# Kernel tuning notes

Hardware: AMD Instinct MI355X
Metric: run time of the kernel (lower is better)

Reference implementation:

```python
import jax, jax.numpy as jnp
import numpy as np
import math

N = 65536   # number of tree nodes
K = 4       # branching factor of the complete K-ary tree
D = 300     # input_size
H = 256     # hidden_size

def _levels(n, k):
    # complete k-ary tree: level l spans [start, start + k**l)
    levels, start, size = [], 0, 1
    while start < n:
        end = min(start + size, n)
        levels.append((start, end))
        start, size = end, size * k
    return levels

LEVELS = _levels(N, K)

def setup_inputs() -> dict:
    key = jax.random.key(0)
    ks = jax.random.split(key, 16)
    def U(k, shape, s):
        return jax.random.uniform(k, shape, jnp.float32, -s, s)
    s1 = 1.0 / math.sqrt(D + H)
    sfi = 1.0 / math.sqrt(D)
    sfh = 1.0 / math.sqrt(H)
    return {
        "inputs": jax.random.normal(ks[0], (N, D), jnp.float32),
        "ix_w": U(ks[1], (H, D), s1), "ix_b": U(ks[2], (H,), s1),
        "ih_w": U(ks[3], (H, H), s1), "ih_b": U(ks[4], (H,), s1),
        "ux_w": U(ks[5], (H, D), s1), "ux_b": U(ks[6], (H,), s1),
        "uh_w": U(ks[7], (H, H), s1), "uh_b": U(ks[8], (H,), s1),
        "fi_w": U(ks[9], (H, D), sfi), "fi_b": U(ks[10], (H,), sfi),
        "fh_w": U(ks[11], (H, H), sfh), "fh_b": U(ks[12], (H,), sfh),
    }

def reference(inputs, ix_w, ix_b, ih_w, ih_b, ux_w, ux_b, uh_w, uh_b,
              fi_w, fi_b, fh_w, fh_b):
    # Precompute all input projections once (batched over every node).
    ix = inputs @ ix_w.T + ix_b   # [N, H]
    ux = inputs @ ux_w.T + ux_b   # [N, H]
    fi = inputs @ fi_w.T + fi_b   # [N, H]
    h = jnp.zeros((N, H), inputs.dtype)
    c = jnp.zeros((N, H), inputs.dtype)
    # Bottom-up over tree levels (children before parents); level bounds static.
    for (s, e) in reversed(LEVELS):
        node = jnp.arange(s, e)                                   # [L]
        cidx = node[:, None] * K + 1 + jnp.arange(K)[None, :]     # [L, K]
        valid = cidx < N
        cidx = jnp.where(valid, cidx, 0)
        m = valid[..., None].astype(inputs.dtype)                 # [L, K, 1]
        hc = h[cidx] * m                                          # [L, K, H]
        cc = c[cidx] * m
        h_sum = hc.sum(axis=1)                                    # [L, H]
        # per-child forget gate: sigmoid(W_fi x + b_fi + W_fh h_k + b_fh)
        f = jax.nn.sigmoid(fi[s:e][:, None, :]
                           + jnp.einsum('lkh,gh->lkg', hc, fh_w) + fh_b)
        fc = (f * cc).sum(axis=1)                                 # masked via cc
        i = jax.nn.sigmoid(ix[s:e] + h_sum @ ih_w.T + ih_b)
        u = jnp.tanh(ux[s:e] + h_sum @ uh_w.T + uh_b)
        c_new = i * u + fc
        h_new = jnp.tanh(c_new)          # no output gate in this module
        h = h.at[s:e].set(h_new)
        c = c.at[s:e].set(c_new)
    # root node state (matches (next_h, [next_h, next_c]) at the root)
    return h[0], c[0]
```

## Files before the change

### kernel.cpp

```cpp
#include <hip/hip_runtime.h>


#define NTOT 65536
#define DD   300
#define KP   320
#define HH   256
#define LEAF_START 16384

typedef unsigned short u16;
typedef unsigned int   u32;
typedef __attribute__((ext_vector_type(8))) short bf16x8;
typedef __attribute__((ext_vector_type(4))) float f32x4;

#define OFF_HB    0ull
#define OFF_C     33554944ull
#define OFF_PRE   100664832ull
#define OFF_WXB   125830656ull
#define OFF_WHB   126322176ull
#define OFF_UNION 126715392ull
#define OFF_XB    (OFF_UNION)
#define OFF_PIU   (OFF_UNION)
#define OFF_PF    (OFF_UNION + 11272192ull)
#define OFF_HSUM  (OFF_UNION + 33685504ull)

__device__ __forceinline__ float sigm(float x) { return 1.f / (1.f + __expf(-x)); }
__device__ __forceinline__ float ftanh(float x) {
    x = fminf(15.f, fmaxf(-15.f, x));
    float e = __expf(2.f * x);
    return (e - 1.f) / (e + 1.f);
}
__device__ __forceinline__ u16 f2bf(float f) {
    union { float f; u32 u; } v; v.f = f;
    u32 r = v.u + 0x7fffu + ((v.u >> 16) & 1u);
    return (u16)(r >> 16);
}
__device__ __forceinline__ float bf2f(u16 b) {
    union { u32 u; float f; } v; v.u = ((u32)b) << 16;
    return v.f;
}

__global__ __launch_bounds__(256) void zero_pad(u16* __restrict__ hb,
                                                float* __restrict__ c) {
    const int t = threadIdx.x;
    hb[(size_t)NTOT * HH + t] = 0;
    c [(size_t)NTOT * HH + t] = 0.f;
}

__global__ __launch_bounds__(256) void conv_x(const float* __restrict__ X,
                                              u32* __restrict__ Xb2) {
    const size_t total = (size_t)NTOT * (KP / 2);
    for (size_t id = (size_t)blockIdx.x * 256 + threadIdx.x; id < total;
         id += (size_t)gridDim.x * 256) {
        const int node = (int)(id / (KP / 2));
        const int k    = ((int)(id % (KP / 2))) * 2;
        const float f0 = (k < DD)     ? X[(size_t)node * DD + k]     : 0.f;
        const float f1 = (k + 1 < DD) ? X[(size_t)node * DD + k + 1] : 0.f;
        Xb2[id] = (u32)f2bf(f0) | ((u32)f2bf(f1) << 16);
    }
}

__global__ __launch_bounds__(256) void conv_wx(const float* __restrict__ ixw,
                                               const float* __restrict__ uxw,
                                               const float* __restrict__ fiw,
                                               u32* __restrict__ W2) {
    const int total = 768 * (KP / 2);
    for (int id = blockIdx.x * 256 + threadIdx.x; id < total;
         id += gridDim.x * 256) {
        const int row = id / (KP / 2);
        const int k   = (id % (KP / 2)) * 2;
        const float* src = (row < 256) ? (ixw + (size_t)row * DD)
                         : (row < 512) ? (uxw + (size_t)(row - 256) * DD)
                                       : (fiw + (size_t)(row - 512) * DD);
        const float f0 = (k < DD)     ? src[k]     : 0.f;
        const float f1 = (k + 1 < DD) ? src[k + 1] : 0.f;
        W2[id] = (u32)f2bf(f0) | ((u32)f2bf(f1) << 16);
    }
}

__global__ __launch_bounds__(256) void conv_wh(const float* __restrict__ ihw,
                                               const float* __restrict__ uhw,
                                               const float* __restrict__ fhw,
                                               u32* __restrict__ W2) {
    const int total = 768 * (HH / 2);
    for (int id = blockIdx.x * 256 + threadIdx.x; id < total;
         id += gridDim.x * 256) {
        const int row = id / (HH / 2);
        const int k   = (id % (HH / 2)) * 2;
        const float* src = (row < 256) ? (ihw + (size_t)row * HH)
                         : (row < 512) ? (uhw + (size_t)(row - 256) * HH)
                                       : (fhw + (size_t)(row - 512) * HH);
        W2[id] = (u32)f2bf(src[k]) | ((u32)f2bf(src[k + 1]) << 16);
    }
}

__global__ __launch_bounds__(256) void leaf_gemm(
    const u16* __restrict__ Xb, const u16* __restrict__ Wxb,
    const float* __restrict__ ixb, const float* __restrict__ ihb,
    const float* __restrict__ uxb, const float* __restrict__ uhb,
    u16* __restrict__ hb, float* __restrict__ c)
{
    __shared__ bf16x8 Ash[64 * 8];
    __shared__ bf16x8 Bsh[128 * 8];

    const int tid  = threadIdx.x;
    const int lane = tid & 63;
    const int w    = tid >> 6;
    const int m16  = lane & 15;
    const int q    = lane >> 4;

    const int row0 = LEAF_START + blockIdx.x * 64;
    const int n0   = blockIdx.y * 64;

    const bf16x8* __restrict__ Xv = (const bf16x8*)Xb;
    const bf16x8* __restrict__ Wv = (const bf16x8*)Wxb;

    f32x4 accI[4], accU[4];
    #pragma unroll
    for (int nf = 0; nf < 4; ++nf) { accI[nf] = (f32x4)0.f; accU[nf] = (f32x4)0.f; }

    const int ar = (w << 4) | m16;

    for (int kt = 0; kt < 5; ++kt) {
        __syncthreads();
        #pragma unroll
        for (int i = 0; i < 2; ++i) {
            const int G = tid + i * 256;
            const int r = G >> 3, g = G & 7;
            Ash[(r << 3) | (g ^ (r & 7))] = Xv[(size_t)(row0 + r) * 40 + kt * 8 + g];
        }
        #pragma unroll
        for (int i = 0; i < 4; ++i) {
            const int G = tid + i * 256;
            const int br = G >> 3, g = G & 7;
            const int nsrc = ((br >> 6) << 8) + n0 + (br & 63);
            Bsh[(br << 3) | (g ^ (br & 7))] = Wv[(size_t)nsrc * 40 + kt * 8 + g];
        }
        __syncthreads();

        #pragma unroll
        for (int ks = 0; ks < 2; ++ks) {
            const int kg = ks * 4 + q;
            const bf16x8 a = Ash[(ar << 3) | (kg ^ (ar & 7))];
            #pragma unroll
            for (int nf = 0; nf < 4; ++nf) {
                const int bri = nf * 16 + m16;
                const bf16x8 bI = Bsh[(bri << 3) | (kg ^ (bri & 7))];
                accI[nf] = __builtin_amdgcn_mfma_f32_16x16x32_bf16(a, bI, accI[nf], 0, 0, 0);
                const int bru = 64 + nf * 16 + m16;
                const bf16x8 bU = Bsh[(bru << 3) | (kg ^ (bru & 7))];
                accU[nf] = __builtin_amdgcn_mfma_f32_16x16x32_bf16(a, bU, accU[nf], 0, 0, 0);
            }
        }
    }

    const int node0 = row0 + (w << 4) + (q << 2);
    #pragma unroll
    for (int nf = 0; nf < 4; ++nf) {
        const int col = n0 + (nf << 4) + m16;
        const float bi = ixb[col] + ihb[col];
        const float bu = uxb[col] + uhb[col];
        #pragma unroll
        for (int r = 0; r < 4; ++r) {
            const float cn = sigm(accI[nf][r] + bi) * ftanh(accU[nf][r] + bu);
            const size_t off = (size_t)(node0 + r) * HH + col;
            c [off] = cn;
            hb[off] = f2bf(ftanh(cn));
        }
    }
}

__global__ __launch_bounds__(256) void proj_gemm(const u16* __restrict__ Xb,
                                                 const u16* __restrict__ Wxb,
                                                 u16* __restrict__ pre)
{
    __shared__ bf16x8 Ash[64 * 8];
    __shared__ bf16x8 Bsh[128 * 8];

    const int tid  = threadIdx.x;
    const int lane = tid & 63;
    const int w    = tid >> 6;
    const int m16  = lane & 15;
    const int q    = lane >> 4;

    const int row0 = blockIdx.x * 64;
    const int n0   = blockIdx.y * 128;

    const bf16x8* __restrict__ Xv = (const bf16x8*)Xb;
    const bf16x8* __restrict__ Wv = (const bf16x8*)Wxb;

    f32x4 acc[8];
    #pragma unroll
    for (int nf = 0; nf < 8; ++nf) acc[nf] = (f32x4)0.f;

    const int ar = (w << 4) | m16;

    for (int kt = 0; kt < 5; ++kt) {
        __syncthreads();
        #pragma unroll
        for (int i = 0; i < 2; ++i) {
            const int G = tid + i * 256;
            const int r = G >> 3, g = G & 7;
            Ash[(r << 3) | (g ^ (r & 7))] = Xv[(size_t)(row0 + r) * 40 + kt * 8 + g];
        }
        #pragma unroll
        for (int i = 0; i < 4; ++i) {
            const int G = tid + i * 256;
            const int br = G >> 3, g = G & 7;
            Bsh[(br << 3) | (g ^ (br & 7))] = Wv[(size_t)(n0 + br) * 40 + kt * 8 + g];
        }
        __syncthreads();

        #pragma unroll
        for (int ks = 0; ks < 2; ++ks) {
            const int kg = ks * 4 + q;
            const bf16x8 a = Ash[(ar << 3) | (kg ^ (ar & 7))];
            #pragma unroll
            for (int nf = 0; nf < 8; ++nf) {
                const int bri = nf * 16 + m16;
                const bf16x8 b = Bsh[(bri << 3) | (kg ^ (bri & 7))];
                acc[nf] = __builtin_amdgcn_mfma_f32_16x16x32_bf16(a, b, acc[nf], 0, 0, 0);
            }
        }
    }

    const int node0 = row0 + (w << 4) + (q << 2);
    #pragma unroll
    for (int nf = 0; nf < 8; ++nf) {
        const int col = n0 + (nf << 4) + m16;
        #pragma unroll
        for (int r = 0; r < 4; ++r)
            pre[(size_t)(node0 + r) * 768 + col] = f2bf(acc[nf][r]);
    }
}

__global__ __launch_bounds__(256) void hsum_kernel(const u16* __restrict__ hb,
                                                   u16* __restrict__ hsumb,
                                                   int crow0, int L)
{
    const int id = blockIdx.x * 256 + threadIdx.x;
    if (id >= L * 64) return;
    const int nloc = id >> 6;
    const int cu   = (id & 63) << 1;
    const u32* __restrict__ src = (const u32*)hb;
    float s0 = 0.f, s1 = 0.f, s2 = 0.f, s3 = 0.f;
    #pragma unroll
    for (int k = 0; k < 4; ++k) {
        const size_t ro = (size_t)(crow0 + 4 * nloc + k) * (HH / 2) + cu;
        const u32 a = src[ro], b = src[ro + 1];
        s0 += bf2f((u16)(a & 0xffff)); s1 += bf2f((u16)(a >> 16));
        s2 += bf2f((u16)(b & 0xffff)); s3 += bf2f((u16)(b >> 16));
    }
    u32* __restrict__ dst = (u32*)hsumb;
    const size_t oo = (size_t)nloc * (HH / 2) + cu;
    dst[oo]     = (u32)f2bf(s0) | ((u32)f2bf(s1) << 16);
    dst[oo + 1] = (u32)f2bf(s2) | ((u32)f2bf(s3) << 16);
}

__global__ __launch_bounds__(256) void rec_gemm(const u16* __restrict__ hb,
                                                const u16* __restrict__ hsumb,
                                                const u16* __restrict__ Whb,
                                                u16* __restrict__ projIU,
                                                u16* __restrict__ projF,
                                                int crow0, int L)
{
    __shared__ bf16x8 Ash[64 * 8];
    __shared__ bf16x8 Bsh[128 * 8];

    const int nIUrb = (L + 63) >> 6;
    const int bid   = blockIdx.x;

    const u16* Aptr; u16* out;
    int ostride, Brow0, orow0, ocol0;
    if (bid < nIUrb * 4) {
        const int rb = bid >> 2, cb = bid & 3;
        Aptr = hsumb + (size_t)rb * 64 * HH;
        out = projIU; ostride = 512; orow0 = rb * 64;
        ocol0 = cb * 128; Brow0 = cb * 128;
    } else {
        const int b2 = bid - nIUrb * 4;
        const int rb = b2 >> 1, cb = b2 & 1;
        Aptr = hb + (size_t)(crow0 + rb * 64) * HH;
        out = projF; ostride = 256; orow0 = rb * 64;
        ocol0 = cb * 128; Brow0 = 512 + cb * 128;
    }

    const int tid  = threadIdx.x;
    const int lane = tid & 63;
    const int w    = tid >> 6;
    const int m16  = lane & 15;
    const int q    = lane >> 4;

    const bf16x8* __restrict__ Av = (const bf16x8*)Aptr;
    const bf16x8* __restrict__ Wv = (const bf16x8*)Whb;

    f32x4 acc[8];
    #pragma unroll
    for (int nf = 0; nf < 8; ++nf) acc[nf] = (f32x4)0.f;

    const int ar = (w << 4) | m16;

    for (int kt = 0; kt < 4; ++kt) {
        __syncthreads();
        #pragma unroll
        for (int i = 0; i < 2; ++i) {
            const int G = tid + i * 256;
            const int r = G >> 3, g = G & 7;
            Ash[(r << 3) | (g ^ (r & 7))] = Av[(size_t)r * 32 + kt * 8 + g];
        }
        #pragma unroll
        for (int i = 0; i < 4; ++i) {
            const int G = tid + i * 256;
            const int br = G >> 3, g = G & 7;
            Bsh[(br << 3) | (g ^ (br & 7))] = Wv[(size_t)(Brow0 + br) * 32 + kt * 8 + g];
        }
        __syncthreads();

        #pragma unroll
        for (int ks = 0; ks < 2; ++ks) {
            const int kg = ks * 4 + q;
            const bf16x8 a = Ash[(ar << 3) | (kg ^ (ar & 7))];
            #pragma unroll
            for (int nf = 0; nf < 8; ++nf) {
                const int bri = nf * 16 + m16;
                const bf16x8 b = Bsh[(bri << 3) | (kg ^ (bri & 7))];
                acc[nf] = __builtin_amdgcn_mfma_f32_16x16x32_bf16(a, b, acc[nf], 0, 0, 0);
            }
        }
    }

    const int r0 = orow0 + (w << 4) + (q << 2);
    #pragma unroll
    for (int nf = 0; nf < 8; ++nf) {
        const int col = ocol0 + (nf << 4) + m16;
        #pragma unroll
        for (int r = 0; r < 4; ++r)
            out[(size_t)(r0 + r) * ostride + col] = f2bf(acc[nf][r]);
    }
}

__global__ __launch_bounds__(256) void gate_kernel(
    const u16* __restrict__ pre, const u16* __restrict__ projIU,
    const u16* __restrict__ projF,
    const float* __restrict__ ixb, const float* __restrict__ ihb,
    const float* __restrict__ uxb, const float* __restrict__ uhb,
    const float* __restrict__ fib, const float* __restrict__ fhb,
    u16* __restrict__ hb, float* __restrict__ c, float* __restrict__ out,
    int s, int crow0)
{
    const int nloc = blockIdx.x;
    const int j    = threadIdx.x;
    const int n    = s + nloc;

    const float aI = bf2f(pre[(size_t)n * 768 + j]) + ixb[j] + ihb[j]
                   + bf2f(projIU[(size_t)nloc * 512 + j]);
    const float aU = bf2f(pre[(size_t)n * 768 + 256 + j]) + uxb[j] + uhb[j]
                   + bf2f(projIU[(size_t)nloc * 512 + 256 + j]);
    const float fpre = bf2f(pre[(size_t)n * 768 + 512 + j]) + fib[j] + fhb[j];

    float fc = 0.f;
    #pragma unroll
    for (int k = 0; k < 4; ++k) {
        const float fg = sigm(fpre + bf2f(projF[(size_t)(4 * nloc + k) * 256 + j]));
        fc = fmaf(fg, c[(size_t)(crow0 + 4 * nloc + k) * HH + j], fc);
    }
    const float cn = fmaf(sigm(aI), ftanh(aU), fc);
    const float hn = ftanh(cn);
    hb[(size_t)n * HH + j] = f2bf(hn);
    c [(size_t)n * HH + j] = cn;
    if (n == 0) { out[j] = hn; out[HH + j] = cn; }
}

extern "C" void kernel_launch(void* const* d_in, const int* in_sizes, int n_in,
                              void* d_out, int out_size, void* d_ws, size_t ws_size,
                              hipStream_t stream) {
    const float* X   = (const float*)d_in[0];
    const float* ixw = (const float*)d_in[1];
    const float* ixb = (const float*)d_in[2];
    const float* ihw = (const float*)d_in[3];
    const float* ihb = (const float*)d_in[4];
    const float* uxw = (const float*)d_in[5];
    const float* uxb = (const float*)d_in[6];
    const float* uhw = (const float*)d_in[7];
    const float* uhb = (const float*)d_in[8];
    const float* fiw = (const float*)d_in[9];
    const float* fib = (const float*)d_in[10];
    const float* fhw = (const float*)d_in[11];
    const float* fhb = (const float*)d_in[12];
    float* out = (float*)d_out;

    char* ws = (char*)d_ws;
    u16*   hb    = (u16*)(ws + OFF_HB);
    float* cbuf  = (float*)(ws + OFF_C);
    u16*   pre   = (u16*)(ws + OFF_PRE);
    u16*   Wxb   = (u16*)(ws + OFF_WXB);
    u16*   Whb   = (u16*)(ws + OFF_WHB);
    u16*   Xb    = (u16*)(ws + OFF_XB);
    u16*   pIU   = (u16*)(ws + OFF_PIU);
    u16*   pF    = (u16*)(ws + OFF_PF);
    u16*   hsumb = (u16*)(ws + OFF_HSUM);

    zero_pad<<<1, 256, 0, stream>>>(hb, cbuf);
    conv_x <<<2048, 256, 0, stream>>>(X, (u32*)Xb);
    conv_wx<<<480, 256, 0, stream>>>(ixw, uxw, fiw, (u32*)Wxb);
    conv_wh<<<384, 256, 0, stream>>>(ihw, uhw, fhw, (u32*)Whb);

    leaf_gemm<<<dim3(768, 4), 256, 0, stream>>>(Xb, Wxb, ixb, ihb, uxb, uhb, hb, cbuf);
    proj_gemm<<<dim3(256, 6), 256, 0, stream>>>(Xb, Wxb, pre);

    const int starts[8] = {5461, 1365, 341, 85, 21, 5, 1, 0};
    const int ends[8]   = {16384, 5461, 1365, 341, 85, 21, 5, 1};
    for (int l = 0; l < 8; ++l) {
        const int s = starts[l], e = ends[l];
        const int L = e - s;
        const int crow0 = 4 * s + 1;
        const int nIUrb = (L + 63) >> 6;
        const int nFrb  = (4 * L + 63) >> 6;
        hsum_kernel<<<(L * 64 + 255) / 256, 256, 0, stream>>>(hb, hsumb, crow0, L);
        rec_gemm<<<nIUrb * 4 + nFrb * 2, 256, 0, stream>>>(hb, hsumb, Whb, pIU, pF, crow0, L);
        gate_kernel<<<L, 256, 0, stream>>>(pre, pIU, pF,
            ixb, ihb, uxb, uhb, fib, fhb, hb, cbuf, out, s, crow0);
    }
}
```

Before: 219.6 us.

## Fuse X bf16 conversion into GEMM loads and enlarge tiles to 128x128

Drops the separate conv_x pass and has leaf_gemm and proj_gemm read fp32 inputs directly, converting them to bf16 while staging to LDS. This saves a full write and re-read of the converted input matrix. All three GEMMs now use 128x128 block tiles with a 2x2 wave layout (4x4 MFMA fragments per wave) for more operand reuse. The leaf GEMM interleaves I/U weight rows and pairs lanes with a shuffle for the epilogue. In exchange, register pressure rises and fewer blocks are launched, and rec_gemm clamps padded rows to the zero pad row.

New measurement: 255.6 us. 16.4% more time.

```diff
diff --git a/kernel.cpp b/kernel.cpp
--- a/kernel.cpp
+++ b/kernel.cpp
@@ -11,6 +11,8 @@
 typedef unsigned int   u32;
 typedef __attribute__((ext_vector_type(8))) short bf16x8;
 typedef __attribute__((ext_vector_type(4))) float f32x4;
+
+union BF8 { bf16x8 v; u16 u[8]; };
 
 #define OFF_HB    0ull
 #define OFF_C     33554944ull
@@ -18,7 +20,6 @@
 #define OFF_WXB   125830656ull
 #define OFF_WHB   126322176ull
 #define OFF_UNION 126715392ull
-#define OFF_XB    (OFF_UNION)
 #define OFF_PIU   (OFF_UNION)
 #define OFF_PF    (OFF_UNION + 11272192ull)
 #define OFF_HSUM  (OFF_UNION + 33685504ull)
@@ -38,25 +39,13 @@
     union { u32 u; float f; } v; v.u = ((u32)b) << 16;
     return v.f;
 }
+__device__ __forceinline__ int lidx(int r, int g) { return (r << 3) | (g ^ (r & 7)); }
 
 __global__ __launch_bounds__(256) void zero_pad(u16* __restrict__ hb,
                                                 float* __restrict__ c) {
     const int t = threadIdx.x;
     hb[(size_t)NTOT * HH + t] = 0;
     c [(size_t)NTOT * HH + t] = 0.f;
-}
-
-__global__ __launch_bounds__(256) void conv_x(const float* __restrict__ X,
-                                              u32* __restrict__ Xb2) {
-    const size_t total = (size_t)NTOT * (KP / 2);
-    for (size_t id = (size_t)blockIdx.x * 256 + threadIdx.x; id < total;
-         id += (size_t)gridDim.x * 256) {
-        const int node = (int)(id / (KP / 2));
-        const int k    = ((int)(id % (KP / 2))) * 2;
-        const float f0 = (k < DD)     ? X[(size_t)node * DD + k]     : 0.f;
-        const float f1 = (k + 1 < DD) ? X[(size_t)node * DD + k + 1] : 0.f;
-        Xb2[id] = (u32)f2bf(f0) | ((u32)f2bf(f1) << 16);
-    }
 }
 
 __global__ __launch_bounds__(256) void conv_wx(const float* __restrict__ ixw,
@@ -93,143 +82,187 @@
     }
 }
 
+__device__ __forceinline__ bf16x8 load_x_granule(const float* __restrict__ src,
+                                                 int k) {
+    BF8 pk;
+    if (k + 8 <= DD) {
+        const float4 f0 = *(const float4*)(src + k);
+        const float4 f1 = *(const float4*)(src + k + 4);
+        pk.u[0] = f2bf(f0.x); pk.u[1] = f2bf(f0.y);
+        pk.u[2] = f2bf(f0.z); pk.u[3] = f2bf(f0.w);
+        pk.u[4] = f2bf(f1.x); pk.u[5] = f2bf(f1.y);
+        pk.u[6] = f2bf(f1.z); pk.u[7] = f2bf(f1.w);
+    } else if (k < DD) {
+        const float4 f0 = *(const float4*)(src + k);
+        pk.u[0] = f2bf(f0.x); pk.u[1] = f2bf(f0.y);
+        pk.u[2] = f2bf(f0.z); pk.u[3] = f2bf(f0.w);
+        pk.u[4] = 0; pk.u[5] = 0; pk.u[6] = 0; pk.u[7] = 0;
+    } else {
+        #pragma unroll
+        for (int j = 0; j < 8; ++j) pk.u[j] = 0;
+    }
+    return pk.v;
+}
+
 __global__ __launch_bounds__(256) void leaf_gemm(
-    const u16* __restrict__ Xb, const u16* __restrict__ Wxb,
+    const float* __restrict__ X, const u16* __restrict__ Wxb,
     const float* __restrict__ ixb, const float* __restrict__ ihb,
     const float* __restrict__ uxb, const float* __restrict__ uhb,
     u16* __restrict__ hb, float* __restrict__ c)
 {
-    __shared__ bf16x8 Ash[64 * 8];
-    __shared__ bf16x8 Bsh[128 * 8];
+    __shared__ bf16x8 Ash[1024];
+    __shared__ bf16x8 Bsh[1024];
 
     const int tid  = threadIdx.x;
     const int lane = tid & 63;
     const int w    = tid >> 6;
-    const int m16  = lane & 15;
-    const int q    = lane >> 4;
-
-    const int row0 = LEAF_START + blockIdx.x * 64;
-    const int n0   = blockIdx.y * 64;
-
-    const bf16x8* __restrict__ Xv = (const bf16x8*)Xb;
+    const int wr   = w >> 1, wc = w & 1;
+    const int m16  = lane & 15, q = lane >> 4;
+
+    const int row0   = LEAF_START + blockIdx.x * 128;
+    const int chbase = blockIdx.y * 64;
+
     const bf16x8* __restrict__ Wv = (const bf16x8*)Wxb;
 
-    f32x4 accI[4], accU[4];
-    #pragma unroll
-    for (int nf = 0; nf < 4; ++nf) { accI[nf] = (f32x4)0.f; accU[nf] = (f32x4)0.f; }
-
-    const int ar = (w << 4) | m16;
+    f32x4 acc[4][4];
+    #pragma unroll
+    for (int mf = 0; mf < 4; ++mf)
+        #pragma unroll
+        for (int nf = 0; nf < 4; ++nf) acc[mf][nf] = (f32x4)0.f;
 
     for (int kt = 0; kt < 5; ++kt) {
         __syncthreads();
         #pragma unroll
-        for (int i = 0; i < 2; ++i) {
+        for (int i = 0; i < 4; ++i) {
             const int G = tid + i * 256;
             const int r = G >> 3, g = G & 7;
-            Ash[(r << 3) | (g ^ (r & 7))] = Xv[(size_t)(row0 + r) * 40 + kt * 8 + g];
+            const int k = kt * 64 + g * 8;
+            Ash[lidx(r, g)] = load_x_granule(X + (size_t)(row0 + r) * DD, k);
         }
         #pragma unroll
         for (int i = 0; i < 4; ++i) {
             const int G = tid + i * 256;
             const int br = G >> 3, g = G & 7;
-            const int nsrc = ((br >> 6) << 8) + n0 + (br & 63);
-            Bsh[(br << 3) | (g ^ (br & 7))] = Wv[(size_t)nsrc * 40 + kt * 8 + g];
+            const int ch = chbase + (br >> 1);
+            const int srow = ch + ((br & 1) << 8);
+            Bsh[lidx(br, g)] = Wv[(size_t)srow * 40 + kt * 8 + g];
         }
         __syncthreads();
 
         #pragma unroll
         for (int ks = 0; ks < 2; ++ks) {
             const int kg = ks * 4 + q;
-            const bf16x8 a = Ash[(ar << 3) | (kg ^ (ar & 7))];
-            #pragma unroll
-            for (int nf = 0; nf < 4; ++nf) {
-                const int bri = nf * 16 + m16;
-                const bf16x8 bI = Bsh[(bri << 3) | (kg ^ (bri & 7))];
-                accI[nf] = __builtin_amdgcn_mfma_f32_16x16x32_bf16(a, bI, accI[nf], 0, 0, 0);
-                const int bru = 64 + nf * 16 + m16;
-                const bf16x8 bU = Bsh[(bru << 3) | (kg ^ (bru & 7))];
-                accU[nf] = __builtin_amdgcn_mfma_f32_16x16x32_bf16(a, bU, accU[nf], 0, 0, 0);
+            bf16x8 a[4], b[4];
+            #pragma unroll
+            for (int mf = 0; mf < 4; ++mf)
+                a[mf] = Ash[lidx(wr * 64 + mf * 16 + m16, kg)];
+            #pragma unroll
+            for (int nf = 0; nf < 4; ++nf)
+                b[nf] = Bsh[lidx(wc * 64 + nf * 16 + m16, kg)];
+            #pragma unroll
+            for (int mf = 0; mf < 4; ++mf)
+                #pragma unroll
+                for (int nf = 0; nf < 4; ++nf)
+                    acc[mf][nf] = __builtin_amdgcn_mfma_f32_16x16x32_bf16(
+                        a[mf], b[nf], acc[mf][nf], 0, 0, 0);
+        }
+    }
+
+    const bool evn = (m16 & 1) == 0;
+    #pragma unroll
+    for (int nf = 0; nf < 4; ++nf) {
+        const int ch = chbase + wc * 32 + nf * 8 + (m16 >> 1);
+        const float bi = ixb[ch] + ihb[ch];
+        const float bu = uxb[ch] + uhb[ch];
+        #pragma unroll
+        for (int mf = 0; mf < 4; ++mf) {
+            #pragma unroll
+            for (int r4 = 0; r4 < 4; ++r4) {
+                const float mine = acc[mf][nf][r4];
+                const float oth  = __shfl_xor(mine, 1, 64);
+                const float aI = evn ? mine : oth;
+                const float aU = evn ? oth : mine;
+                const float cn = sigm(aI + bi) * ftanh(aU + bu);
+                const int node = row0 + wr * 64 + mf * 16 + q * 4 + r4;
+                const size_t off = (size_t)node * HH + ch;
+                if (evn) c[off] = cn;
+                else     hb[off] = f2bf(ftanh(cn));
             }
         }
     }
-
-    const int node0 = row0 + (w << 4) + (q << 2);
-    #pragma unroll
-    for (int nf = 0; nf < 4; ++nf) {
-        const int col = n0 + (nf << 4) + m16;
-        const float bi = ixb[col] + ihb[col];
-        const float bu = uxb[col] + uhb[col];
-        #pragma unroll
-        for (int r = 0; r < 4; ++r) {
-            const float cn = sigm(accI[nf][r] + bi) * ftanh(accU[nf][r] + bu);
-            const size_t off = (size_t)(node0 + r) * HH + col;
-            c [off] = cn;
-            hb[off] = f2bf(ftanh(cn));
-        }
-    }
-}
-
-__global__ __launch_bounds__(256) void proj_gemm(const u16* __restrict__ Xb,
+}
+
+__global__ __launch_bounds__(256) void proj_gemm(const float* __restrict__ X,
                                                  const u16* __restrict__ Wxb,
                                                  u16* __restrict__ pre)
 {
-    __shared__ bf16x8 Ash[64 * 8];
-    __shared__ bf16x8 Bsh[128 * 8];
+    __shared__ bf16x8 Ash[1024];
+    __shared__ bf16x8 Bsh[1024];
 
     const int tid  = threadIdx.x;
     const int lane = tid & 63;
     const int w    = tid >> 6;
-    const int m16  = lane & 15;
-    const int q    = lane >> 4;
-
-    const int row0 = blockIdx.x * 64;
+    const int wr   = w >> 1, wc = w & 1;
+    const int m16  = lane & 15, q = lane >> 4;
+
+    const int row0 = blockIdx.x * 128;
     const int n0   = blockIdx.y * 128;
 
-    const bf16x8* __restrict__ Xv = (const bf16x8*)Xb;
     const bf16x8* __restrict__ Wv = (const bf16x8*)Wxb;
 
-    f32x4 acc[8];
-    #pragma unroll
-    for (int nf = 0; nf < 8; ++nf) acc[nf] = (f32x4)0.f;
-
-    const int ar = (w << 4) | m16;
+    f32x4 acc[4][4];
+    #pragma unroll
+    for (int mf = 0; mf < 4; ++mf)
+        #pragma unroll
+        for (int nf = 0; nf < 4; ++nf) acc[mf][nf] = (f32x4)0.f;
 
     for (int kt = 0; kt < 5; ++kt) {
         __syncthreads();
         #pragma unroll
-        for (int i = 0; i < 2; ++i) {
+        for (int i = 0; i < 4; ++i) {
             const int G = tid + i * 256;
             const int r = G >> 3, g = G & 7;
-            Ash[(r << 3) | (g ^ (r & 7))] = Xv[(size_t)(row0 + r) * 40 + kt * 8 + g];
+            const int k = kt * 64 + g * 8;
+            Ash[lidx(r, g)] = load_x_granule(X + (size_t)(row0 + r) * DD, k);
         }
         #pragma unroll
         for (int i = 0; i < 4; ++i) {
             const int G = tid + i * 256;
             const int br = G >> 3, g = G & 7;
-            Bsh[(br << 3) | (g ^ (br & 7))] = Wv[(size_t)(n0 + br) * 40 + kt * 8 + g];
+            Bsh[lidx(br, g)] = Wv[(size_t)(n0 + br) * 40 + kt * 8 + g];
         }
         __syncthreads();
 
         #pragma unroll
         for (int ks = 0; ks < 2; ++ks) {
             const int kg = ks * 4 + q;
-            const bf16x8 a = Ash[(ar << 3) | (kg ^ (ar & 7))];
-            #pragma unroll
-            for (int nf = 0; nf < 8; ++nf) {
-                const int bri = nf * 16 + m16;
-                const bf16x8 b = Bsh[(bri << 3) | (kg ^ (bri & 7))];
-                acc[nf] = __builtin_amdgcn_mfma_f32_16x16x32_bf16(a, b, acc[nf], 0, 0, 0);
+            bf16x8 a[4], b[4];
+            #pragma unroll
+            for (int mf = 0; mf < 4; ++mf)
+                a[mf] = Ash[lidx(wr * 64 + mf * 16 + m16, kg)];
+            #pragma unroll
+            for (int nf = 0; nf < 4; ++nf)
+                b[nf] = Bsh[lidx(wc * 64 + nf * 16 + m16, kg)];
+            #pragma unroll
+            for (int mf = 0; mf < 4; ++mf)
+                #pragma unroll
+                for (int nf = 0; nf < 4; ++nf)
+                    acc[mf][nf] = __builtin_amdgcn_mfma_f32_16x16x32_bf16(
+                        a[mf], b[nf], acc[mf][nf], 0, 0, 0);
+        }
+    }
+
+    #pragma unroll
+    for (int mf = 0; mf < 4; ++mf) {
+        #pragma unroll
+        for (int nf = 0; nf < 4; ++nf) {
+            const int col = n0 + wc * 64 + nf * 16 + m16;
+            #pragma unroll
+            for (int r4 = 0; r4 < 4; ++r4) {
+                const int node = row0 + wr * 64 + mf * 16 + q * 4 + r4;
+                pre[(size_t)node * 768 + col] = f2bf(acc[mf][nf][r4]);
             }
         }
-    }
-
-    const int node0 = row0 + (w << 4) + (q << 2);
-    #pragma unroll
-    for (int nf = 0; nf < 8; ++nf) {
-        const int col = n0 + (nf << 4) + m16;
-        #pragma unroll
-        for (int r = 0; r < 4; ++r)
-            pre[(size_t)(node0 + r) * 768 + col] = f2bf(acc[nf][r]);
     }
 }
 
@@ -263,78 +296,85 @@
                                                 u16* __restrict__ projF,
                                                 int crow0, int L)
 {
-    __shared__ bf16x8 Ash[64 * 8];
-    __shared__ bf16x8 Bsh[128 * 8];
-
-    const int nIUrb = (L + 63) >> 6;
+    __shared__ bf16x8 Ash[1024];
+    __shared__ bf16x8 Bsh[1024];
+
+    const int nIUrb = (L + 127) >> 7;
     const int bid   = blockIdx.x;
 
-    const u16* Aptr; u16* out;
-    int ostride, Brow0, orow0, ocol0;
-    if (bid < nIUrb * 4) {
-        const int rb = bid >> 2, cb = bid & 3;
-        Aptr = hsumb + (size_t)rb * 64 * HH;
-        out = projIU; ostride = 512; orow0 = rb * 64;
-        ocol0 = cb * 128; Brow0 = cb * 128;
-    } else {
-        const int b2 = bid - nIUrb * 4;
-        const int rb = b2 >> 1, cb = b2 & 1;
-        Aptr = hb + (size_t)(crow0 + rb * 64) * HH;
-        out = projF; ostride = 256; orow0 = rb * 64;
-        ocol0 = cb * 128; Brow0 = 512 + cb * 128;
-    }
+    bool isIU; int rb, cb;
+    if (bid < nIUrb * 4) { isIU = true;  rb = bid >> 2; cb = bid & 3; }
+    else { isIU = false; const int b2 = bid - nIUrb * 4; rb = b2 >> 1; cb = b2 & 1; }
+
+    const int row0  = rb * 128;
+    const int Brow0 = isIU ? cb * 128 : 512 + cb * 128;
+    const int ocol0 = cb * 128;
+    u16* __restrict__ out = isIU ? projIU : projF;
+    const int ostride = isIU ? 512 : 256;
 
     const int tid  = threadIdx.x;
     const int lane = tid & 63;
     const int w    = tid >> 6;
-    const int m16  = lane & 15;
-    const int q    = lane >> 4;
-
-    const bf16x8* __restrict__ Av = (const bf16x8*)Aptr;
+    const int wr   = w >> 1, wc = w & 1;
+    const int m16  = lane & 15, q = lane >> 4;
+
+    const bf16x8* __restrict__ Av = isIU ? (const bf16x8*)hsumb : (const bf16x8*)hb;
     const bf16x8* __restrict__ Wv = (const bf16x8*)Whb;
 
-    f32x4 acc[8];
-    #pragma unroll
-    for (int nf = 0; nf < 8; ++nf) acc[nf] = (f32x4)0.f;
-
-    const int ar = (w << 4) | m16;
+    f32x4 acc[4][4];
+    #pragma unroll
+    for (int mf = 0; mf < 4; ++mf)
+        #pragma unroll
+        for (int nf = 0; nf < 4; ++nf) acc[mf][nf] = (f32x4)0.f;
 
     for (int kt = 0; kt < 4; ++kt) {
         __syncthreads();
         #pragma unroll
-        for (int i = 0; i < 2; ++i) {
+        for (int i = 0; i < 4; ++i) {
             const int G = tid + i * 256;
             const int r = G >> 3, g = G & 7;
-            Ash[(r << 3) | (g ^ (r & 7))] = Av[(size_t)r * 32 + kt * 8 + g];
+            int srow = row0 + r;
+            if (!isIU) { srow = crow0 + srow; if (srow > NTOT) srow = NTOT; }
+            Ash[lidx(r, g)] = Av[(size_t)srow * 32 + kt * 8 + g];
         }
         #pragma unroll
         for (int i = 0; i < 4; ++i) {
             const int G = tid + i * 256;
             const int br = G >> 3, g = G & 7;
-            Bsh[(br << 3) | (g ^ (br & 7))] = Wv[(size_t)(Brow0 + br) * 32 + kt * 8 + g];
+            Bsh[lidx(br, g)] = Wv[(size_t)(Brow0 + br) * 32 + kt * 8 + g];
         }
         __syncthreads();
 
         #pragma unroll
         for (int ks = 0; ks < 2; ++ks) {
             const int kg = ks * 4 + q;
-            const bf16x8 a = Ash[(ar << 3) | (kg ^ (ar & 7))];
-            #pragma unroll
-            for (int nf = 0; nf < 8; ++nf) {
-                const int bri = nf * 16 + m16;
-                const bf16x8 b = Bsh[(bri << 3) | (kg ^ (bri & 7))];
-                acc[nf] = __builtin_amdgcn_mfma_f32_16x16x32_bf16(a, b, acc[nf], 0, 0, 0);
+            bf16x8 a[4], b[4];
+            #pragma unroll
+            for (int mf = 0; mf < 4; ++mf)
+                a[mf] = Ash[lidx(wr * 64 + mf * 16 + m16, kg)];
+            #pragma unroll
+            for (int nf = 0; nf < 4; ++nf)
+                b[nf] = Bsh[lidx(wc * 64 + nf * 16 + m16, kg)];
+            #pragma unroll
+            for (int mf = 0; mf < 4; ++mf)
+                #pragma unroll
+                for (int nf = 0; nf < 4; ++nf)
+                    acc[mf][nf] = __builtin_amdgcn_mfma_f32_16x16x32_bf16(
+                        a[mf], b[nf], acc[mf][nf], 0, 0, 0);
+        }
+    }
+
+    #pragma unroll
+    for (int mf = 0; mf < 4; ++mf) {
+        #pragma unroll
+        for (int nf = 0; nf < 4; ++nf) {
+            const int col = ocol0 + wc * 64 + nf * 16 + m16;
+            #pragma unroll
+            for (int r4 = 0; r4 < 4; ++r4) {
+                const int orow = row0 + wr * 64 + mf * 16 + q * 4 + r4;
+                out[(size_t)orow * ostride + col] = f2bf(acc[mf][nf][r4]);
             }
         }
-    }
-
-    const int r0 = orow0 + (w << 4) + (q << 2);
-    #pragma unroll
-    for (int nf = 0; nf < 8; ++nf) {
-        const int col = ocol0 + (nf << 4) + m16;
-        #pragma unroll
-        for (int r = 0; r < 4; ++r)
-            out[(size_t)(r0 + r) * ostride + col] = f2bf(acc[nf][r]);
     }
 }
 
@@ -394,18 +434,16 @@
     u16*   pre   = (u16*)(ws + OFF_PRE);
     u16*   Wxb   = (u16*)(ws + OFF_WXB);
     u16*   Whb   = (u16*)(ws + OFF_WHB);
-    u16*   Xb    = (u16*)(ws + OFF_XB);
     u16*   pIU   = (u16*)(ws + OFF_PIU);
     u16*   pF    = (u16*)(ws + OFF_PF);
     u16*   hsumb = (u16*)(ws + OFF_HSUM);
 
     zero_pad<<<1, 256, 0, stream>>>(hb, cbuf);
-    conv_x <<<2048, 256, 0, stream>>>(X, (u32*)Xb);
     conv_wx<<<480, 256, 0, stream>>>(ixw, uxw, fiw, (u32*)Wxb);
     conv_wh<<<384, 256, 0, stream>>>(ihw, uhw, fhw, (u32*)Whb);
 
-    leaf_gemm<<<dim3(768, 4), 256, 0, stream>>>(Xb, Wxb, ixb, ihb, uxb, uhb, hb, cbuf);
-    proj_gemm<<<dim3(256, 6), 256, 0, stream>>>(Xb, Wxb, pre);
+    leaf_gemm<<<dim3(384, 4), 256, 0, stream>>>(X, Wxb, ixb, ihb, uxb, uhb, hb, cbuf);
+    proj_gemm<<<dim3(128, 6), 256, 0, stream>>>(X, Wxb, pre);
 
     const int starts[8] = {5461, 1365, 341, 85, 21, 5, 1, 0};
     const int ends[8]   = {16384, 5461, 1365, 341, 85, 21, 5, 1};
@@ -413,8 +451,8 @@
         const int s = starts[l], e = ends[l];
         const int L = e - s;
         const int crow0 = 4 * s + 1;
-        const int nIUrb = (L + 63) >> 6;
-        const int nFrb  = (4 * L + 63) >> 6;
+        const int nIUrb = (L + 127) >> 7;
+        const int nFrb  = (4 * L + 127) >> 7;
         hsum_kernel<<<(L * 64 + 255) / 256, 256, 0, stream>>>(hb, hsumb, crow0, L);
         rec_gemm<<<nIUrb * 4 + nFrb * 2, 256, 0, stream>>>(hb, hsumb, Whb, pIU, pF, crow0, L);
         gate_kernel<<<L, 256, 0, stream>>>(pre, pIU, pF,
```
